# Performance work log

Hardware: AMD Instinct MI355X
Metric: run time of the kernel (lower is better)

Reference implementation:

```python
import jax, jax.numpy as jnp
import numpy as np

NUM_HEADS = 16

def setup_inputs() -> dict:
    key = jax.random.key(0)
    ks = jax.random.split(key, 12)
    B, NQ, NK = 4, 1024, 1024
    DQ = DK = DV = 1024
    AH = 1024   # num_heads * head_dim
    OUT = 1024
    s = lambda d: 1.0 / np.sqrt(d)
    return {
        "q": jax.random.normal(ks[0], (B, NQ, DQ), jnp.float32),
        "k": jax.random.normal(ks[1], (B, NK, DK), jnp.float32),
        "v": jax.random.normal(ks[2], (B, NK, DV), jnp.float32),
        "attn_mask": jnp.ones((NQ, NK), jnp.float32),
        "Wq": jax.random.normal(ks[3], (DQ, AH), jnp.float32) * s(DQ),
        "bq": jnp.zeros((AH,), jnp.float32),
        "Wk": jax.random.normal(ks[4], (DK, AH), jnp.float32) * s(DK),
        "bk": jnp.zeros((AH,), jnp.float32),
        "Wv": jax.random.normal(ks[5], (DV, AH), jnp.float32) * s(DV),
        "bv": jnp.zeros((AH,), jnp.float32),
        "Wo": jax.random.normal(ks[6], (AH, OUT), jnp.float32) * s(AH),
        "bo": jnp.zeros((OUT,), jnp.float32),
    }

def reference(q, k, v, attn_mask, Wq, bq, Wk, bk, Wv, bv, Wo, bo):
    b, n_q, _ = q.shape
    n_k = k.shape[1]
    all_head_dim = Wq.shape[1]
    scale = all_head_dim ** (-0.5)  # NOTE: module scales by all_head_dim, not head_dim

    # module reshapes as (b, n, head_dim, num_heads): heads are the LAST axis
    def split_heads(x):
        return x.reshape(b, x.shape[1], -1, NUM_HEADS).transpose(0, 3, 1, 2)  # (b,H,n,d)

    qh = split_heads(q @ Wq + bq) * scale
    kh = split_heads(k @ Wk + bk)
    vh = split_heads(v @ Wv + bv)

    attn = jnp.einsum('bhqd,bhkd->bhqk', qh, kh)
    attn = attn - 100000000.0 * (1.0 - attn_mask[None, None, :, :])
    attn = jax.nn.softmax(attn, axis=-1)

    o = jnp.einsum('bhqk,bhkd->bhqd', attn, vh)
    o = o.transpose(0, 2, 3, 1).reshape(b, n_q, -1)  # (b,n_q,head_dim*H)
    return o @ Wo + bo
```

## Files before the change

### kernel.cpp

```cpp
#include <hip/hip_runtime.h>
#include <stdint.h>

typedef __attribute__((ext_vector_type(8))) short short8;
typedef __attribute__((ext_vector_type(8))) unsigned short ushort8;
typedef __attribute__((ext_vector_type(4))) float f32x4;
typedef unsigned short u16;
typedef unsigned int u32;

__device__ __forceinline__ u16 f2bf(float f){
  u32 u = __builtin_bit_cast(u32, f);
  u32 r = (u + 0x7fffu + ((u >> 16) & 1u)) >> 16;
  return (u16)r;
}

__device__ __forceinline__ u32 cvtpk(float lo, float hi){
  u32 r;
  asm("v_cvt_pk_bf16_f32 %0, %1, %2" : "=v"(r) : "v"(lo), "v"(hi));
  return r;
}

__device__ __forceinline__ void gload16(const void* g, void* l){
  __builtin_amdgcn_global_load_lds((const __attribute__((address_space(1))) void*)g,
                                   (__attribute__((address_space(3))) void*)l, 16, 0, 0);
}

__global__ void prep_kernel(const float* __restrict__ q, const float* __restrict__ k,
                            const float* __restrict__ v, u16* __restrict__ xq,
                            u16* __restrict__ xk, u16* __restrict__ xv,
                            const float* __restrict__ Wq, const float* __restrict__ Wk,
                            const float* __restrict__ Wv, const float* __restrict__ Wo,
                            u16* __restrict__ WqT, u16* __restrict__ WkT,
                            u16* __restrict__ WvT, u16* __restrict__ WoT){
  __shared__ float t[64][65];
  int bid = blockIdx.x;
  int tid = threadIdx.x;
  if (bid < 2048){
    const int NV8 = 4194304 / 8;
    for (int i = bid * 256 + tid; i < 3 * NV8; i += 2048 * 256){
      int tt = i / NV8, r = i - tt * NV8;
      const float4* src = (const float4*)(tt == 0 ? q : (tt == 1 ? k : v));
      u16* dst = (tt == 0 ? xq : (tt == 1 ? xk : xv));
      float4 f0 = src[r * 2], f1 = src[r * 2 + 1];
      ushort8 o;
      o[0] = f2bf(f0.x); o[1] = f2bf(f0.y); o[2] = f2bf(f0.z); o[3] = f2bf(f0.w);
      o[4] = f2bf(f1.x); o[5] = f2bf(f1.y); o[6] = f2bf(f1.z); o[7] = f2bf(f1.w);
      *(ushort8*)(dst + r * 8) = o;
    }
  } else {
    int idx = bid - 2048;
    int bx = idx & 15, by = (idx >> 4) & 15, z = idx >> 8;
    const float* src = (z == 0 ? Wq : (z == 1 ? Wk : (z == 2 ? Wv : Wo)));
    u16* dst = (z == 0 ? WqT : (z == 1 ? WkT : (z == 2 ? WvT : WoT)));
    int c0 = by * 64;
    #pragma unroll
    for (int p = 0; p < 4; ++p){
      int rl = p * 16 + (tid >> 4);
      int srcRow = (z < 3) ? (bx * 64 + rl) : (rl * 16 + bx);
      float4 f = *(const float4*)(src + srcRow * 1024 + c0 + (tid & 15) * 4);
      t[rl][(tid & 15) * 4 + 0] = f.x;
      t[rl][(tid & 15) * 4 + 1] = f.y;
      t[rl][(tid & 15) * 4 + 2] = f.z;
      t[rl][(tid & 15) * 4 + 3] = f.w;
    }
    __syncthreads();
    int ro = tid >> 2;
    int kc = (tid & 3) * 16;
    int outBase = (c0 + ro) * 1024 + bx * 64;
    #pragma unroll
    for (int j = 0; j < 16; ++j)
      dst[outBase + kc + j] = f2bf(t[kc + j][ro]);
  }
}

__global__ void maskflag_kernel(const float* __restrict__ mask, u32* __restrict__ flags){
  int q0 = blockIdx.x * 128, k0 = blockIdx.y * 64;
  int tid = threadIdx.x;
  bool ok = true;
  #pragma unroll
  for (int p = 0; p < 8; ++p){
    int fi = p * 256 + tid;
    int r = fi >> 4, c = (fi & 15) * 4;
    float4 f = *(const float4*)(mask + (size_t)(q0 + r) * 1024 + k0 + c);
    ok = ok && (f.x == 1.0f) && (f.y == 1.0f) && (f.z == 1.0f) && (f.w == 1.0f);
  }
  __shared__ int s_ok[4];
  unsigned long long b = __ballot(ok);
  if ((tid & 63) == 0) s_ok[tid >> 6] = (b == ~0ull) ? 1 : 0;
  __syncthreads();
  if (tid == 0)
    flags[blockIdx.x * 16 + blockIdx.y] = (u32)(s_ok[0] & s_ok[1] & s_ok[2] & s_ok[3]);
}

struct QkvArgs {
  const u16* A[3]; const u16* BT[3]; const float* bias[3];
  u16* outQ; u16* outK; u16* outVT;
};

__global__ __launch_bounds__(256, 4)
void gemm_qkv_kernel(QkvArgs args){
  __shared__ __align__(16) u16 As[2][128 * 32];
  __shared__ __align__(16) u16 Bs[2][128 * 32];
  int wg = blockIdx.x;
  int l  = (wg & 7) * 96 + (wg >> 3);
  int z  = l >> 8;
  int rem = l & 255;
  int m0 = (rem >> 3) * 128, n0 = (rem & 7) * 128;
  const u16* __restrict__ A  = args.A[z];
  const u16* __restrict__ BT = args.BT[z];
  const float* __restrict__ bias = args.bias[z];
  int tid = threadIdx.x, w = tid >> 6, lane = tid & 63, lr = lane & 15, lg = lane >> 4;
  int wr = w >> 1, wc = w & 1;
  f32x4 acc[4][4];
  #pragma unroll
  for (int i = 0; i < 4; ++i)
    #pragma unroll
    for (int j = 0; j < 4; ++j)
      acc[i][j] = f32x4{0.f, 0.f, 0.f, 0.f};

  auto stage = [&](int kt, int b){
    int k0 = kt * 32;
    #pragma unroll
    for (int p = 0; p < 2; ++p){
      int chunk = p * 4096 + w * 1024;
      int L = chunk + lane * 16;
      int row = L >> 6, inrow = L & 63;
      int srcB = inrow ^ (((row >> 1) & 3) << 4);
      gload16(A + (m0 + row) * 1024 + k0 + (srcB >> 1), (char*)As[b] + chunk);
      gload16(BT + (n0 + row) * 1024 + k0 + (srcB >> 1), (char*)Bs[b] + chunk);
    }
  };
  stage(0, 0);

  for (int kt = 0; kt < 32; ++kt){
    int cur = kt & 1;
    if (kt < 31){
      stage(kt + 1, cur ^ 1);
      asm volatile("s_waitcnt vmcnt(4)" ::: "memory");
    } else {
      asm volatile("s_waitcnt vmcnt(0)" ::: "memory");
    }
    __builtin_amdgcn_s_barrier();

    short8 af[4], bfr[4];
    int cb = lg * 16;
    #pragma unroll
    for (int i = 0; i < 4; ++i){
      int ra = wr * 64 + i * 16 + lr;
      af[i] = *(const short8*)((const char*)As[cur] + ra * 64 + (cb ^ (((ra >> 1) & 3) << 4)));
      int rb = wc * 64 + i * 16 + lr;
      bfr[i] = *(const short8*)((const char*)Bs[cur] + rb * 64 + (cb ^ (((rb >> 1) & 3) << 4)));
    }
    #pragma unroll
    for (int i = 0; i < 4; ++i)
      #pragma unroll
      for (int j = 0; j < 4; ++j)
        acc[i][j] = __builtin_amdgcn_mfma_f32_16x16x32_bf16(af[i], bfr[j], acc[i][j], 0, 0, 0);

    __builtin_amdgcn_s_barrier();
  }

  float bv[4];
  #pragma unroll
  for (int j = 0; j < 4; ++j) bv[j] = bias[n0 + wc * 64 + j * 16 + lr];
  float scale = (z == 0) ? 0.0450842200f : 1.0f;
  int bb = m0 >> 10;
  int dd0 = (n0 + wc * 64) >> 4;
  if (z == 2){
    #pragma unroll
    for (int i = 0; i < 4; ++i){
      int nn0 = (m0 + wr * 64 + i * 16 + lg * 4) & 1023;
      #pragma unroll
      for (int j = 0; j < 4; ++j){
        uint2 pw;
        pw.x = cvtpk(acc[i][j][0] + bv[j], acc[i][j][1] + bv[j]);
        pw.y = cvtpk(acc[i][j][2] + bv[j], acc[i][j][3] + bv[j]);
        *(uint2*)(args.outVT + ((size_t)(bb * 16 + lr) * 64 + dd0 + j) * 1024 + nn0) = pw;
      }
    }
  } else {
    u16* o = (z == 0) ? args.outQ : args.outK;
    #pragma unroll
    for (int i = 0; i < 4; ++i){
      #pragma unroll
      for (int rr = 0; rr < 4; ++rr){
        int nn = (m0 + wr * 64 + i * 16 + lg * 4 + rr) & 1023;
        uint2 pw;
        pw.x = cvtpk((acc[i][0][rr] + bv[0]) * scale, (acc[i][1][rr] + bv[1]) * scale);
        pw.y = cvtpk((acc[i][2][rr] + bv[2]) * scale, (acc[i][3][rr] + bv[3]) * scale);
        *(uint2*)(o + ((size_t)(bb * 16 + lr) * 1024 + nn) * 64 + dd0) = pw;
      }
    }
  }
}

__global__ __launch_bounds__(256, 3)
void attn_kernel(const u16* __restrict__ Qh, const u16* __restrict__ Kh,
                 const u16* __restrict__ VT, const float* __restrict__ mask,
                 const u32* __restrict__ flags, u16* __restrict__ Oh){
  __shared__ __align__(16) u16 PQs[128 * 72];
  __shared__ __align__(16) u16 Ks[2][64 * 64];
  __shared__ __align__(16) u16 Vs[2][64 * 64];
  u16* Qs = PQs;
  u16* Ps = PQs;
  int tid = threadIdx.x, w = tid >> 6, lane = tid & 63, lr = lane & 15, lg = lane >> 4;
  int wg = blockIdx.x;
  int idx = wg >> 3;
  int bh = (wg & 7) * 8 + (idx >> 3);
  int qt = idx & 7;
  int q0 = qt * 128;
  const u16* Qb = Qh + (size_t)bh * 65536;
  const u16* Kb = Kh + (size_t)bh * 65536;
  const u16* Vb = VT + (size_t)bh * 65536;

  u32 fbits = 0;
  #pragma unroll
  for (int t = 0; t < 16; ++t) fbits |= (flags[qt * 16 + t] & 1u) << t;

  #pragma unroll
  for (int r = 0; r < 4; ++r){
    int chunk = (r * 4 + w) * 1024;
    int L = chunk + lane * 16;
    int row = L >> 7, inrow = L & 127;
    int srcB = inrow ^ ((row & 7) << 4);
    gload16(Qb + (q0 + row) * 64 + (srcB >> 1), (char*)Qs + chunk);
  }

  auto stage_kv = [&](int t, int b){
    int kn = t * 64;
    #pragma unroll
    for (int r = 0; r < 2; ++r){
      int chunk = (r * 4 + w) * 1024;
      int L = chunk + lane * 16;
      int row = L >> 7, inrow = L & 127;
      int srcB = inrow ^ ((row & 7) << 4);
      gload16(Kb + (kn + row) * 64 + (srcB >> 1), (char*)Ks[b] + chunk);
      gload16(Vb + row * 1024 + kn + (srcB >> 1), (char*)Vs[b] + chunk);
    }
  };
  stage_kv(0, 0);

  asm volatile("s_waitcnt vmcnt(4)" ::: "memory");
  __builtin_amdgcn_s_barrier();
  short8 qreg[2][2];
  #pragma unroll
  for (int i = 0; i < 2; ++i)
    #pragma unroll
    for (int kh = 0; kh < 2; ++kh){
      int ra = w * 32 + i * 16 + lr;
      qreg[i][kh] = *(const short8*)((const char*)Qs + ra * 128 +
                                     ((kh * 64 + lg * 16) ^ ((ra & 7) << 4)));
    }
  asm volatile("s_waitcnt lgkmcnt(0)" ::: "memory");

  f32x4 o[2][4];
  float m_run[2], l_run[2];
  m_run[0] = m_run[1] = -3.0e38f;
  l_run[0] = l_run[1] = 0.f;
  #pragma unroll
  for (int i = 0; i < 2; ++i)
    #pragma unroll
    for (int j = 0; j < 4; ++j)
      o[i][j] = f32x4{0.f, 0.f, 0.f, 0.f};

  for (int kt = 0; kt < 16; ++kt){
    int cur = kt & 1;
    int kn0 = kt * 64;

    f32x4 s[2][4];
    if (fbits & (1u << kt)){
      #pragma unroll
      for (int i = 0; i < 2; ++i)
        #pragma unroll
        for (int j = 0; j < 4; ++j)
          s[i][j] = f32x4{0.f, 0.f, 0.f, 0.f};
    } else {
      #pragma unroll
      for (int i = 0; i < 2; ++i){
        int qg = q0 + w * 32 + i * 16 + lr;
        #pragma unroll
        for (int j = 0; j < 4; ++j){
          int kg = kn0 + j * 16 + lg * 4;
          float4 mm = *(const float4*)(mask + (size_t)qg * 1024 + kg);
          s[i][j][0] = fmaf(1.44269504e8f, mm.x, -1.44269504e8f);
          s[i][j][1] = fmaf(1.44269504e8f, mm.y, -1.44269504e8f);
          s[i][j][2] = fmaf(1.44269504e8f, mm.z, -1.44269504e8f);
          s[i][j][3] = fmaf(1.44269504e8f, mm.w, -1.44269504e8f);
        }
      }
    }

    if (kt < 15){
      stage_kv(kt + 1, cur ^ 1);
      asm volatile("s_waitcnt vmcnt(4)" ::: "memory");
    } else {
      asm volatile("s_waitcnt vmcnt(0)" ::: "memory");
    }
    __builtin_amdgcn_s_barrier();

    #pragma unroll
    for (int kh = 0; kh < 2; ++kh){
      short8 kf[4];
      int cb = kh * 64 + lg * 16;
      #pragma unroll
      for (int j = 0; j < 4; ++j){
        int rb = j * 16 + lr;
        kf[j] = *(const short8*)((const char*)Ks[cur] + rb * 128 + (cb ^ ((rb & 7) << 4)));
      }
      #pragma unroll
      for (int i = 0; i < 2; ++i)
        #pragma unroll
        for (int j = 0; j < 4; ++j)
          s[i][j] = __builtin_amdgcn_mfma_f32_16x16x32_bf16(kf[j], qreg[i][kh], s[i][j], 0, 0, 0);
    }

    float alpha[2];
    bool need[2];
    #pragma unroll
    for (int i = 0; i < 2; ++i){
      float m0a = fmaxf(fmaxf(s[i][0][0], s[i][0][1]), fmaxf(s[i][0][2], s[i][0][3]));
      float m1a = fmaxf(fmaxf(s[i][1][0], s[i][1][1]), fmaxf(s[i][1][2], s[i][1][3]));
      float m2a = fmaxf(fmaxf(s[i][2][0], s[i][2][1]), fmaxf(s[i][2][2], s[i][2][3]));
      float m3a = fmaxf(fmaxf(s[i][3][0], s[i][3][1]), fmaxf(s[i][3][2], s[i][3][3]));
      float mx = fmaxf(fmaxf(m0a, m1a), fmaxf(m2a, m3a));
      mx = fmaxf(mx, __shfl_xor(mx, 16));
      mx = fmaxf(mx, __shfl_xor(mx, 32));
      need[i] = __any(mx > m_run[i] + 8.0f);
      float mnew;
      if (need[i]){
        mnew = fmaxf(m_run[i], mx);
        alpha[i] = exp2f(m_run[i] - mnew);
        m_run[i] = mnew;
      } else {
        mnew = m_run[i];
        alpha[i] = 1.0f;
      }
      float rs = 0.f;
      #pragma unroll
      for (int j = 0; j < 4; ++j)
        #pragma unroll
        for (int rr = 0; rr < 4; ++rr){
          float p = exp2f(s[i][j][rr] - mnew);
          s[i][j][rr] = p;
          rs += p;
        }
      rs += __shfl_xor(rs, 16);
      rs += __shfl_xor(rs, 32);
      l_run[i] = need[i] ? (l_run[i] * alpha[i] + rs) : (l_run[i] + rs);
      int prow = w * 32 + i * 16 + lr;
      #pragma unroll
      for (int j = 0; j < 4; ++j){
        uint2 pw;
        pw.x = cvtpk(s[i][j][0], s[i][j][1]);
        pw.y = cvtpk(s[i][j][2], s[i][j][3]);
        *(uint2*)(Ps + prow * 72 + j * 16 + lg * 4) = pw;
      }
    }

    #pragma unroll
    for (int i = 0; i < 2; ++i)
      if (need[i]){
        #pragma unroll
        for (int jd = 0; jd < 4; ++jd)
          #pragma unroll
          for (int rr = 0; rr < 4; ++rr)
            o[i][jd][rr] *= alpha[i];
      }

    #pragma unroll
    for (int kh = 0; kh < 2; ++kh){
      short8 pf[2], vf[4];
      int cb = kh * 64 + lg * 16;
      #pragma unroll
      for (int i = 0; i < 2; ++i){
        int ra = w * 32 + i * 16 + lr;
        pf[i] = *(const short8*)((const char*)Ps + ra * 144 + cb);
      }
      #pragma unroll
      for (int jd = 0; jd < 4; ++jd){
        int rb = jd * 16 + lr;
        vf[jd] = *(const short8*)((const char*)Vs[cur] + rb * 128 + (cb ^ ((rb & 7) << 4)));
      }
      #pragma unroll
      for (int i = 0; i < 2; ++i)
        #pragma unroll
        for (int jd = 0; jd < 4; ++jd)
          o[i][jd] = __builtin_amdgcn_mfma_f32_16x16x32_bf16(vf[jd], pf[i], o[i][jd], 0, 0, 0);
    }
    __builtin_amdgcn_s_barrier();
  }

  #pragma unroll
  for (int i = 0; i < 2; ++i){
    float inv = 1.0f / l_run[i];
    int qg = q0 + w * 32 + i * 16 + lr;
    #pragma unroll
    for (int jd = 0; jd < 4; ++jd){
      uint2 ov;
      ov.x = cvtpk(o[i][jd][0] * inv, o[i][jd][1] * inv);
      ov.y = cvtpk(o[i][jd][2] * inv, o[i][jd][3] * inv);
      *(uint2*)(Oh + ((size_t)bh * 1024 + qg) * 64 + jd * 16 + lg * 4) = ov;
    }
  }
}

__global__ __launch_bounds__(256, 4)
void gemm_out_kernel(const u16* __restrict__ Oh, const u16* __restrict__ WoT,
                     const float* __restrict__ bo, float* __restrict__ out){
  __shared__ __align__(16) u16 As[4][128 * 32];
  __shared__ __align__(16) u16 Bs[4][64 * 32];
  int wg = blockIdx.x;
  int l  = (wg & 7) * 64 + (wg >> 3);
  int m0 = (l >> 4) * 128, n0 = (l & 15) * 64;
  int tid = threadIdx.x, w = tid >> 6, lane = tid & 63, lr = lane & 15, lg = lane >> 4;
  int wm = w >> 1, wn = w & 1;
  f32x4 acc[4][2];
  #pragma unroll
  for (int i = 0; i < 4; ++i)
    #pragma unroll
    for (int j = 0; j < 2; ++j)
      acc[i][j] = f32x4{0.f, 0.f, 0.f, 0.f};

  auto stage = [&](int kt, int b){
    int hh = kt >> 1;
    int dofs = (kt & 1) * 32;
    int k0 = kt * 32;
    #pragma unroll
    for (int p = 0; p < 2; ++p){
      int chunk = p * 4096 + w * 1024;
      int L = chunk + lane * 16;
      int row = L >> 6, inrow = L & 63;
      int srcB = inrow ^ (((row >> 1) & 3) << 4);
      int m = m0 + row;
      int bb = m >> 10, nn = m & 1023;
      gload16(Oh + ((size_t)(bb * 16 + hh) * 1024 + nn) * 64 + dofs + (srcB >> 1),
              (char*)As[b] + chunk);
    }
    {
      int chunk = w * 1024;
      int L = chunk + lane * 16;
      int row = L >> 6, inrow = L & 63;
      int srcB = inrow ^ (((row >> 1) & 3) << 4);
      gload16(WoT + (n0 + row) * 1024 + k0 + (srcB >> 1), (char*)Bs[b] + chunk);
    }
  };
  stage(0, 0);
  stage(1, 1);
  stage(2, 2);

  for (int kt = 0; kt < 32; ++kt){
    int cur = kt & 3;
    if (kt <= 29){
      asm volatile("s_waitcnt vmcnt(6)" ::: "memory");
    } else if (kt == 30){
      asm volatile("s_waitcnt vmcnt(3)" ::: "memory");
    } else {
      asm volatile("s_waitcnt vmcnt(0)" ::: "memory");
    }
    __builtin_amdgcn_s_barrier();

    short8 af[4], bfr[2];
    int cb = lg * 16;
    #pragma unroll
    for (int i = 0; i < 4; ++i){
      int ra = wm * 64 + i * 16 + lr;
      af[i] = *(const short8*)((const char*)As[cur] + ra * 64 + (cb ^ (((ra >> 1) & 3) << 4)));
    }
    #pragma unroll
    for (int j = 0; j < 2; ++j){
      int rb = wn * 32 + j * 16 + lr;
      bfr[j] = *(const short8*)((const char*)Bs[cur] + rb * 64 + (cb ^ (((rb >> 1) & 3) << 4)));
    }
    if (kt < 29) stage(kt + 3, (kt + 3) & 3);

    #pragma unroll
    for (int i = 0; i < 4; ++i)
      #pragma unroll
      for (int j = 0; j < 2; ++j)
        acc[i][j] = __builtin_amdgcn_mfma_f32_16x16x32_bf16(af[i], bfr[j], acc[i][j], 0, 0, 0);
  }

  float bv[2];
  #pragma unroll
  for (int j = 0; j < 2; ++j) bv[j] = bo[n0 + wn * 32 + j * 16 + lr];
  #pragma unroll
  for (int i = 0; i < 4; ++i)
    #pragma unroll
    for (int j = 0; j < 2; ++j){
      int gcol = n0 + wn * 32 + j * 16 + lr;
      #pragma unroll
      for (int rr = 0; rr < 4; ++rr){
        int grow = m0 + wm * 64 + i * 16 + lg * 4 + rr;
        out[(size_t)grow * 1024 + gcol] = acc[i][j][rr] + bv[j];
      }
    }
}

extern "C" void kernel_launch(void* const* d_in, const int* in_sizes, int n_in,
                              void* d_out, int out_size, void* d_ws, size_t ws_size,
                              hipStream_t stream){
  const float* q    = (const float*)d_in[0];
  const float* k    = (const float*)d_in[1];
  const float* v    = (const float*)d_in[2];
  const float* mask = (const float*)d_in[3];
  const float* Wq   = (const float*)d_in[4];
  const float* bq   = (const float*)d_in[5];
  const float* Wk   = (const float*)d_in[6];
  const float* bk   = (const float*)d_in[7];
  const float* Wv   = (const float*)d_in[8];
  const float* bv   = (const float*)d_in[9];
  const float* Wo   = (const float*)d_in[10];
  const float* bo   = (const float*)d_in[11];

  char* ws = (char*)d_ws;
  u16* Qh  = (u16*)(ws + (size_t)0);
  u16* Kh  = (u16*)(ws + ((size_t)8  << 20));
  u16* VT  = (u16*)(ws + ((size_t)16 << 20));
  u16* Oh  = (u16*)(ws + ((size_t)24 << 20));
  u16* Xq  = (u16*)(ws + ((size_t)32 << 20));
  u16* Xk  = (u16*)(ws + ((size_t)40 << 20));
  u16* Xv  = (u16*)(ws + ((size_t)48 << 20));
  u16* WqT = (u16*)(ws + ((size_t)56 << 20));
  u16* WkT = (u16*)(ws + ((size_t)58 << 20));
  u16* WvT = (u16*)(ws + ((size_t)60 << 20));
  u16* WoT = (u16*)(ws + ((size_t)62 << 20));
  u32* Flags = (u32*)(ws + ((size_t)32 << 20));

  prep_kernel<<<dim3(3072), dim3(256), 0, stream>>>(q, k, v, Xq, Xk, Xv,
                                                    Wq, Wk, Wv, Wo, WqT, WkT, WvT, WoT);

  QkvArgs a;
  a.A[0] = Xq;  a.A[1] = Xk;  a.A[2] = Xv;
  a.BT[0] = WqT; a.BT[1] = WkT; a.BT[2] = WvT;
  a.bias[0] = bq; a.bias[1] = bk; a.bias[2] = bv;
  a.outQ = Qh; a.outK = Kh; a.outVT = VT;
  gemm_qkv_kernel<<<dim3(768), dim3(256), 0, stream>>>(a);

  maskflag_kernel<<<dim3(8, 16), dim3(256), 0, stream>>>(mask, Flags);
  attn_kernel<<<dim3(512), dim3(256), 0, stream>>>(Qh, Kh, VT, mask, Flags, Oh);
  gemm_out_kernel<<<dim3(512), dim3(256), 0, stream>>>(Oh, WoT, bo, (float*)d_out);
}
```

Baseline: 126.6 us.

## Enlarge QKV GEMM tiles to 256x256 with deep multi-stage LDS pipeline

The QKV projection GEMM moves from 128x128 tiles with 256 threads and double buffering to 256x256 tiles with 512 threads (8 waves), and the grid shrinks from 768 to 192 blocks. Operands stream through a 16-slot LDS ring of 128x32 half-tiles, kept 11 stages ahead with fine-grained vmcnt waits, and MFMA bursts run at raised priority via s_setprio. The aim is more data reuse per global load and better hiding of load latency. In exchange it uses 128KB of LDS per block and only 192 blocks, so CU occupancy and load balance get worse.

```diff
diff --git a/kernel.cpp b/kernel.cpp
--- a/kernel.cpp
+++ b/kernel.cpp
@@ -96,79 +96,89 @@
   u16* outQ; u16* outK; u16* outVT;
 };
 
-__global__ __launch_bounds__(256, 4)
+__global__ __launch_bounds__(512, 2)
 void gemm_qkv_kernel(QkvArgs args){
-  __shared__ __align__(16) u16 As[2][128 * 32];
-  __shared__ __align__(16) u16 Bs[2][128 * 32];
+  __shared__ __align__(16) u16 hs[16 * 4096];
   int wg = blockIdx.x;
-  int l  = (wg & 7) * 96 + (wg >> 3);
-  int z  = l >> 8;
-  int rem = l & 255;
-  int m0 = (rem >> 3) * 128, n0 = (rem & 7) * 128;
+  int l  = (wg & 7) * 24 + (wg >> 3);
+  int z  = l >> 6;
+  int rem = l & 63;
+  int m0 = (rem >> 2) * 256, n0 = (rem & 3) * 256;
   const u16* __restrict__ A  = args.A[z];
   const u16* __restrict__ BT = args.BT[z];
   const float* __restrict__ bias = args.bias[z];
   int tid = threadIdx.x, w = tid >> 6, lane = tid & 63, lr = lane & 15, lg = lane >> 4;
-  int wr = w >> 1, wc = w & 1;
-  f32x4 acc[4][4];
-  #pragma unroll
-  for (int i = 0; i < 4; ++i)
+  int wm = w >> 2, wn = w & 3;
+
+  auto stage = [&](int n){
+    int t = n >> 2, h = n & 3;
+    const u16* src = (h < 2) ? A : BT;
+    int baseRow = ((h < 2) ? m0 : n0) + (h & 1) * 128;
+    int off = tid * 16;
+    int row = off >> 6, inrow = off & 63;
+    int srcB = inrow ^ (((row >> 1) & 3) << 4);
+    gload16(src + (baseRow + row) * 1024 + t * 32 + (srcB >> 1),
+            (char*)hs + (n & 15) * 8192 + off);
+  };
+
+  for (int n = 0; n < 11; ++n) stage(n);
+
+  f32x4 acc[8][4];
+  #pragma unroll
+  for (int i = 0; i < 8; ++i)
     #pragma unroll
     for (int j = 0; j < 4; ++j)
       acc[i][j] = f32x4{0.f, 0.f, 0.f, 0.f};
 
-  auto stage = [&](int kt, int b){
-    int k0 = kt * 32;
-    #pragma unroll
-    for (int p = 0; p < 2; ++p){
-      int chunk = p * 4096 + w * 1024;
-      int L = chunk + lane * 16;
-      int row = L >> 6, inrow = L & 63;
-      int srcB = inrow ^ (((row >> 1) & 3) << 4);
-      gload16(A + (m0 + row) * 1024 + k0 + (srcB >> 1), (char*)As[b] + chunk);
-      gload16(BT + (n0 + row) * 1024 + k0 + (srcB >> 1), (char*)Bs[b] + chunk);
-    }
-  };
-  stage(0, 0);
-
-  for (int kt = 0; kt < 32; ++kt){
-    int cur = kt & 1;
-    if (kt < 31){
-      stage(kt + 1, cur ^ 1);
-      asm volatile("s_waitcnt vmcnt(4)" ::: "memory");
-    } else {
-      asm volatile("s_waitcnt vmcnt(0)" ::: "memory");
-    }
-    __builtin_amdgcn_s_barrier();
-
-    short8 af[4], bfr[4];
-    int cb = lg * 16;
-    #pragma unroll
-    for (int i = 0; i < 4; ++i){
-      int ra = wr * 64 + i * 16 + lr;
-      af[i] = *(const short8*)((const char*)As[cur] + ra * 64 + (cb ^ (((ra >> 1) & 3) << 4)));
-      int rb = wc * 64 + i * 16 + lr;
-      bfr[i] = *(const short8*)((const char*)Bs[cur] + rb * 64 + (cb ^ (((rb >> 1) & 3) << 4)));
-    }
-    #pragma unroll
-    for (int i = 0; i < 4; ++i)
-      #pragma unroll
-      for (int j = 0; j < 4; ++j)
-        acc[i][j] = __builtin_amdgcn_mfma_f32_16x16x32_bf16(af[i], bfr[j], acc[i][j], 0, 0, 0);
-
-    __builtin_amdgcn_s_barrier();
+  short8 bf[4];
+  for (int t = 0; t < 32; ++t){
+    int slotA = ((4 * t + wm) & 15) * 8192;
+    int slotB = ((4 * t + 2 + (wn >> 1)) & 15) * 8192;
+    #pragma unroll
+    for (int p = 0; p < 4; ++p){
+      if (p == 0){
+        if (t < 30)       asm volatile("s_waitcnt vmcnt(7)" ::: "memory");
+        else if (t == 30) asm volatile("s_waitcnt vmcnt(4)" ::: "memory");
+        else              asm volatile("s_waitcnt vmcnt(0)" ::: "memory");
+        __builtin_amdgcn_s_barrier();
+        #pragma unroll
+        for (int j = 0; j < 4; ++j){
+          int rb = (wn & 1) * 64 + j * 16 + lr;
+          bf[j] = *(const short8*)((const char*)hs + slotB + rb * 64 +
+                                   ((lg * 16) ^ (((rb >> 1) & 3) << 4)));
+        }
+      }
+      short8 af[2];
+      #pragma unroll
+      for (int ii = 0; ii < 2; ++ii){
+        int ra = (p * 2 + ii) * 16 + lr;
+        af[ii] = *(const short8*)((const char*)hs + slotA + ra * 64 +
+                                  ((lg * 16) ^ (((ra >> 1) & 3) << 4)));
+      }
+      int P = 4 * t + p;
+      if (P <= 116) stage(P + 11);
+      __builtin_amdgcn_s_setprio(1);
+      #pragma unroll
+      for (int ii = 0; ii < 2; ++ii)
+        #pragma unroll
+        for (int j = 0; j < 4; ++j)
+          acc[p * 2 + ii][j] = __builtin_amdgcn_mfma_f32_16x16x32_bf16(
+              af[ii], bf[j], acc[p * 2 + ii][j], 0, 0, 0);
+      __builtin_amdgcn_s_setprio(0);
+      __builtin_amdgcn_s_barrier();
+    }
   }
 
   float bv[4];
   #pragma unroll
-  for (int j = 0; j < 4; ++j) bv[j] = bias[n0 + wc * 64 + j * 16 + lr];
+  for (int j = 0; j < 4; ++j) bv[j] = bias[n0 + wn * 64 + j * 16 + lr];
   float scale = (z == 0) ? 0.0450842200f : 1.0f;
   int bb = m0 >> 10;
-  int dd0 = (n0 + wc * 64) >> 4;
+  int dd0 = (n0 + wn * 64) >> 4;
   if (z == 2){
     #pragma unroll
-    for (int i = 0; i < 4; ++i){
-      int nn0 = (m0 + wr * 64 + i * 16 + lg * 4) & 1023;
+    for (int i = 0; i < 8; ++i){
+      int nn0 = (m0 + wm * 128 + i * 16 + lg * 4) & 1023;
       #pragma unroll
       for (int j = 0; j < 4; ++j){
         uint2 pw;
@@ -180,10 +190,10 @@
   } else {
     u16* o = (z == 0) ? args.outQ : args.outK;
     #pragma unroll
-    for (int i = 0; i < 4; ++i){
+    for (int i = 0; i < 8; ++i){
       #pragma unroll
       for (int rr = 0; rr < 4; ++rr){
-        int nn = (m0 + wr * 64 + i * 16 + lg * 4 + rr) & 1023;
+        int nn = (m0 + wm * 128 + i * 16 + lg * 4 + rr) & 1023;
         uint2 pw;
         pw.x = cvtpk((acc[i][0][rr] + bv[0]) * scale, (acc[i][1][rr] + bv[1]) * scale);
         pw.y = cvtpk((acc[i][2][rr] + bv[2]) * scale, (acc[i][3][rr] + bv[3]) * scale);
@@ -533,7 +543,7 @@
   a.BT[0] = WqT; a.BT[1] = WkT; a.BT[2] = WvT;
   a.bias[0] = bq; a.bias[1] = bk; a.bias[2] = bv;
   a.outQ = Qh; a.outK = Kh; a.outVT = VT;
-  gemm_qkv_kernel<<<dim3(768), dim3(256), 0, stream>>>(a);
+  gemm_qkv_kernel<<<dim3(192), dim3(512), 0, stream>>>(a);
 
   maskflag_kernel<<<dim3(8, 16), dim3(256), 0, stream>>>(mask, Flags);
   attn_kernel<<<dim3(512), dim3(256), 0, stream>>>(Qh, Kh, VT, mask, Flags, Oh);
```

New measurement: 131.3 us. 1.04x slower.
